# Optimization experiments

Measured on AMD Instinct MI355X. Metric: run time of the kernel, lower is better.

## Reference

```python
import jax, jax.numpy as jnp
import numpy as np
import itertools

NODE_DIM = 30
NUM_FEAT = 64
EDGE_DIM = NODE_DIM * NODE_DIM  # 900
D_IN, HID, LAT = 1024, 2048, 256
OUT_DIM = EDGE_DIM + NODE_DIM * NUM_FEAT  # 2820

_opt_nodes = [20, 21, 22, 23, 24, 25, 26, 27, 28, 29]
_opt_edges = [(i, j) for i, j in itertools.product(_opt_nodes, _opt_nodes) if i <= j]  # 55
_log_nodes = [20, 21, 22, 23, 24, 25, 26, 27, 28, 29, 14, 15]
_log_edges = [(i, j) for i, j in itertools.product(_log_nodes, _log_nodes) if i <= j]  # 78
N_OPT_NODES = len(_opt_nodes)          # 10
N_OPT_EDGES = len(_opt_edges)          # 55
N_LOG_NODES = len(_log_nodes)          # 12 (softmax width; only first 10 applied)
N_LOG_EDGES = len(_log_edges)          # 78 (softmax width; only first 55 applied)
OPT_NODES = jnp.array(_opt_nodes)
E0 = jnp.array([e[0] for e in _opt_edges])
E1 = jnp.array([e[1] for e in _opt_edges])


def _bn(x, g, b, m, v):
    # eval-mode BatchNorm1d, eps=1e-5
    return (x - m) * jax.lax.rsqrt(v + 1e-5) * g + b


def _attn_mlp(x, W1, b1, W2, b2):
    return jnp.tanh(x @ W1 + b1) @ W2 + b2


def _apply_attention(node_repr, edge_repr, node_w, edge_w):
    # softmax over full weight width, but indices always come from the optical lists
    nw = jax.nn.softmax(node_w, axis=1)[:, :N_OPT_NODES]   # [B,10]
    ew = jax.nn.softmax(edge_w, axis=1)[:, :N_OPT_EDGES]   # [B,55]
    node_repr = node_repr.at[:, OPT_NODES, :].set(node_repr[:, OPT_NODES, :] * nw[:, :, None])
    edge_repr = edge_repr.at[:, E0, E1].set(edge_repr[:, E0, E1] * ew)
    return node_repr, edge_repr


def setup_inputs() -> dict:
    key = jax.random.key(0)
    ks = iter(jax.random.split(key, 64))
    B = 8192
    s = 0.02
    def W(shape):
        return jax.random.normal(next(ks), shape, dtype=jnp.float32) * s
    inp = {
        "x": jax.random.normal(next(ks), (B, D_IN), dtype=jnp.float32),
        "optical": jax.random.normal(next(ks), (B, D_IN), dtype=jnp.float32),
        "log": jax.random.normal(next(ks), (B, D_IN), dtype=jnp.float32),
        "enc_W": W((D_IN, HID)), "enc_b": W((HID,)),
        "bn1_g": jnp.ones((HID,)), "bn1_b": jnp.zeros((HID,)),
        "bn1_m": W((HID,)), "bn1_v": jax.random.uniform(next(ks), (HID,)) + 0.5,
        "mu_W": W((HID, LAT)), "mu_b": W((LAT,)),
        "lv_W": W((HID, LAT)), "lv_b": W((LAT,)),
        "dec_W1": W((LAT, HID)), "dec_b1": W((HID,)),
        "bn2_g": jnp.ones((HID,)), "bn2_b": jnp.zeros((HID,)),
        "bn2_m": W((HID,)), "bn2_v": jax.random.uniform(next(ks), (HID,)) + 0.5,
        "dec_W2": W((HID, OUT_DIM)), "dec_b2": W((OUT_DIM,)),
        "on_W1": W((D_IN, D_IN // 2)), "on_b1": W((D_IN // 2,)),
        "on_W2": W((D_IN // 2, N_OPT_NODES)), "on_b2": W((N_OPT_NODES,)),
        "oe_W1": W((D_IN, D_IN // 2)), "oe_b1": W((D_IN // 2,)),
        "oe_W2": W((D_IN // 2, N_OPT_EDGES)), "oe_b2": W((N_OPT_EDGES,)),
        "ln_W1": W((D_IN, D_IN // 2)), "ln_b1": W((D_IN // 2,)),
        "ln_W2": W((D_IN // 2, N_LOG_NODES)), "ln_b2": W((N_LOG_NODES,)),
        "le_W1": W((D_IN, D_IN // 2)), "le_b1": W((D_IN // 2,)),
        "le_W2": W((D_IN // 2, N_LOG_EDGES)), "le_b2": W((N_LOG_EDGES,)),
    }
    return inp


def reference(x, optical, log, enc_W, enc_b, bn1_g, bn1_b, bn1_m, bn1_v,
              mu_W, mu_b, lv_W, lv_b, dec_W1, dec_b1, bn2_g, bn2_b, bn2_m, bn2_v,
              dec_W2, dec_b2, on_W1, on_b1, on_W2, on_b2, oe_W1, oe_b1, oe_W2, oe_b2,
              ln_W1, ln_b1, ln_W2, ln_b2, le_W1, le_b1, le_W2, le_b2):
    # encode (Linear -> ReLU -> BatchNorm(eval) -> Dropout(identity))
    h1 = _bn(jax.nn.relu(x @ enc_W + enc_b), bn1_g, bn1_b, bn1_m, bn1_v)
    mu = h1 @ mu_W + mu_b
    logvar = h1 @ lv_W + lv_b
    z = mu  # eval-mode reparameterize
    # decode
    h2 = _bn(jax.nn.relu(z @ dec_W1 + dec_b1), bn2_g, bn2_b, bn2_m, bn2_v)
    out = h2 @ dec_W2 + dec_b2
    edge_repr = out[:, :EDGE_DIM].reshape(-1, NODE_DIM, NODE_DIM)
    node_repr = out[:, EDGE_DIM:].reshape(-1, NODE_DIM, NUM_FEAT)
    # optical attention
    onw = _attn_mlp(optical, on_W1, on_b1, on_W2, on_b2)
    oew = _attn_mlp(optical, oe_W1, oe_b1, oe_W2, oe_b2)
    node_repr, edge_repr = _apply_attention(node_repr, edge_repr, onw, oew)
    # log attention (wider softmax, same indices — faithful to original code)
    lnw = _attn_mlp(log, ln_W1, ln_b1, ln_W2, ln_b2)
    lew = _attn_mlp(log, le_W1, le_b1, le_W2, le_b2)
    node_repr, edge_repr = _apply_attention(node_repr, edge_repr, lnw, lew)
    return edge_repr, node_repr, mu, logvar
```

## Files before the change

kernel.cpp:

```cpp
#include <hip/hip_runtime.h>

using u16 = unsigned short;
using u32 = unsigned int;

typedef __attribute__((ext_vector_type(8))) short bf16x8;
typedef __attribute__((ext_vector_type(4))) float f32x4;

__device__ __forceinline__ u16 f2bf(float f) {
  u32 u = __float_as_uint(f);
  u += 0x7fffu + ((u >> 16) & 1u);
  return (u16)(u >> 16);
}
__device__ __forceinline__ float bf2f(u16 h) { return __uint_as_float(((u32)h) << 16); }

__device__ __forceinline__ void gld16(const u16* g, u16* s) {
  __builtin_amdgcn_global_load_lds((const __attribute__((address_space(1))) u32*)g,
                                   (__attribute__((address_space(3))) u32*)s, 16, 0, 0);
}

struct EpParams {
  const float* bias;
  const float* bnsc;
  const float* bnsh;
  u16* dhi; u16* dlo; int dstride;
  float* f32a; float* f32b; int f32stride;
  const float* nscale; const float* escale;
};

template<int EP, int NM, bool SLO>
__global__ __launch_bounds__(256, (NM == 1) ? 3 : 2) void gemm_k(
    const u16* __restrict__ Ah, const u16* __restrict__ Al, int lda,
    const u16* __restrict__ Bh, const u16* __restrict__ Bl,
    int K, int N, EpParams p)
{
  __shared__ __align__(16) u16 sAh[4096], sBh[4096];
  __shared__ __align__(16) u16 sAl[(NM >= 2) ? 4096 : 16];
  __shared__ __align__(16) u16 sBl[(NM == 3) ? 4096 : 16];
  const int t = threadIdx.x;
  const int lane = t & 63, wid = t >> 6;
  const int tm = blockIdx.x, tn = blockIdx.y;

  const int rp = t >> 2, sp = t & 3;
  const int rl = (rp & ~1) | ((rp & 1) ^ ((rp >> 2) & 1));
  const int sl = sp ^ (rl & 3);
  const u16* pAh = Ah + (size_t)(tm * 128 + rl) * (size_t)lda + sl * 8;
  const u16* pBh = Bh + (size_t)(tn * 128 + rl) * (size_t)K + sl * 8;
  const u16* pAl = (NM >= 2) ? Al + (size_t)(tm * 128 + rl) * (size_t)lda + sl * 8 : pAh;
  const u16* pBl = (NM == 3) ? Bl + (size_t)(tn * 128 + rl) * (size_t)K + sl * 8 : pBh;
  const size_t aStep = (size_t)64 * (size_t)lda;
  const size_t bStep = (size_t)64 * (size_t)K;

  f32x4 acc[4][4];
#pragma unroll
  for (int m = 0; m < 4; m++)
#pragma unroll
    for (int n = 0; n < 4; n++) acc[m][n] = f32x4{0.f, 0.f, 0.f, 0.f};

  const int fr = lane & 15, fg = lane >> 4;
  const int wm = wid >> 1, wn = wid & 1;

  for (int kk = 0; kk < K; kk += 32) {
    gld16(pAh + kk,          sAh + wid * 512);
    gld16(pAh + aStep + kk,  sAh + 2048 + wid * 512);
    gld16(pBh + kk,          sBh + wid * 512);
    gld16(pBh + bStep + kk,  sBh + 2048 + wid * 512);
    if constexpr (NM >= 2) {
      gld16(pAl + kk,         sAl + wid * 512);
      gld16(pAl + aStep + kk, sAl + 2048 + wid * 512);
    }
    if constexpr (NM == 3) {
      gld16(pBl + kk,         sBl + wid * 512);
      gld16(pBl + bStep + kk, sBl + 2048 + wid * 512);
    }
    __syncthreads();

    bf16x8 a_h[4], b_h[4], a_l[4], b_l[4];
#pragma unroll
    for (int f = 0; f < 4; f++) {
      const int ar = wm * 64 + f * 16 + fr;
      const int br = wn * 64 + f * 16 + fr;
      a_h[f] = *(const bf16x8*)&sAh[(ar * 32 + fg * 8) ^ ((ar & 7) << 3)];
      b_h[f] = *(const bf16x8*)&sBh[(br * 32 + fg * 8) ^ ((br & 7) << 3)];
      if constexpr (NM >= 2) a_l[f] = *(const bf16x8*)&sAl[(ar * 32 + fg * 8) ^ ((ar & 7) << 3)];
      if constexpr (NM == 3) b_l[f] = *(const bf16x8*)&sBl[(br * 32 + fg * 8) ^ ((br & 7) << 3)];
    }
#pragma unroll
    for (int m = 0; m < 4; m++)
#pragma unroll
      for (int n = 0; n < 4; n++) {
        if constexpr (NM == 3)
          acc[m][n] = __builtin_amdgcn_mfma_f32_16x16x32_bf16(a_h[m], b_l[n], acc[m][n], 0, 0, 0);
        if constexpr (NM >= 2)
          acc[m][n] = __builtin_amdgcn_mfma_f32_16x16x32_bf16(a_l[m], b_h[n], acc[m][n], 0, 0, 0);
        acc[m][n] = __builtin_amdgcn_mfma_f32_16x16x32_bf16(a_h[m], b_h[n], acc[m][n], 0, 0, 0);
      }
    __syncthreads();
  }

  const int rowb = tm * 128 + wm * 64;
  const int colb = tn * 128 + wn * 64;
#pragma unroll
  for (int n = 0; n < 4; n++) {
    const int col = colb + n * 16 + fr;
#pragma unroll
    for (int m = 0; m < 4; m++) {
#pragma unroll
      for (int r = 0; r < 4; r++) {
        const int row = rowb + m * 16 + fg * 4 + r;
        float val = acc[m][n][r];
        if constexpr (EP == 0) {
          val += p.bias[col];
          val = fmaxf(val, 0.f);
          val = val * p.bnsc[col] + p.bnsh[col];
          u16 h = f2bf(val);
          p.dhi[(size_t)row * p.dstride + col] = h;
          if constexpr (SLO)
            p.dlo[(size_t)row * p.dstride + col] = f2bf(val - bf2f(h));
        } else if constexpr (EP == 1) {
          val += p.bias[col];
          if (col < 256) {
            p.f32a[(size_t)row * 256 + col] = val;
            u16 h = f2bf(val);
            p.dhi[(size_t)row * 256 + col] = h;
            p.dlo[(size_t)row * 256 + col] = f2bf(val - bf2f(h));
          } else {
            p.f32b[(size_t)row * 256 + (col - 256)] = val;
          }
        } else if constexpr (EP == 2) {
          val = tanhf(val + p.bias[col]);
          p.dhi[(size_t)row * p.dstride + col] = f2bf(val);
        } else if constexpr (EP == 3) {
          if (col < N) p.f32a[(size_t)row * p.f32stride + col] = val + p.bias[col];
        } else {
          if (col < N) {
            val += p.bias[col];
            if (col < 900) {
              int rr = col / 30, cc = col - rr * 30;
              float s = 1.f;
              if (rr >= 20 && cc >= 20 && rr <= cc) {
                int i0 = rr - 20, j0 = cc - 20;
                int k = i0 * 10 - ((i0 * (i0 - 1)) >> 1) + (j0 - i0);
                s = p.escale[(size_t)row * 55 + k];
              }
              p.f32a[(size_t)row * 900 + col] = val * s;
            } else {
              int tc = col - 900, rr = tc >> 6;
              float s = (rr >= 20) ? p.nscale[(size_t)row * 10 + (rr - 20)] : 1.f;
              p.f32b[(size_t)row * 1920 + tc] = val * s;
            }
          }
        }
      }
    }
  }
}

__global__ void conv3(const float* __restrict__ x, const float* __restrict__ opt,
                      const float* __restrict__ lg, u16* __restrict__ xh,
                      u16* __restrict__ xl, u16* __restrict__ oh, u16* __restrict__ lh) {
  const int SEG = 8192 * 1024 / 4;
  int i = blockIdx.x * blockDim.x + threadIdx.x;
  if (i < SEG) {
    float4 v = ((const float4*)x)[i];
    ushort4 hh, ll;
    hh.x = f2bf(v.x); ll.x = f2bf(v.x - bf2f(hh.x));
    hh.y = f2bf(v.y); ll.y = f2bf(v.y - bf2f(hh.y));
    hh.z = f2bf(v.z); ll.z = f2bf(v.z - bf2f(hh.z));
    hh.w = f2bf(v.w); ll.w = f2bf(v.w - bf2f(hh.w));
    ((ushort4*)xh)[i] = hh;
    ((ushort4*)xl)[i] = ll;
  } else if (i < 2 * SEG) {
    int j = i - SEG;
    float4 v = ((const float4*)opt)[j];
    ushort4 hh;
    hh.x = f2bf(v.x); hh.y = f2bf(v.y); hh.z = f2bf(v.z); hh.w = f2bf(v.w);
    ((ushort4*)oh)[j] = hh;
  } else if (i < 3 * SEG) {
    int j = i - 2 * SEG;
    float4 v = ((const float4*)lg)[j];
    ushort4 hh;
    hh.x = f2bf(v.x); hh.y = f2bf(v.y); hh.z = f2bf(v.z); hh.w = f2bf(v.w);
    ((ushort4*)lh)[j] = hh;
  }
}

__global__ void conv_wT(const float* __restrict__ W, u16* __restrict__ Th,
                        u16* __restrict__ Tl, int K, int N) {
  __shared__ float tile[32][33];
  int k0 = blockIdx.x * 32, n0 = blockIdx.y * 32;
  int tx = threadIdx.x, ty = threadIdx.y;
#pragma unroll
  for (int i = ty; i < 32; i += 8) {
    int n = n0 + tx;
    tile[i][tx] = (n < N) ? W[(size_t)(k0 + i) * N + n] : 0.f;
  }
  __syncthreads();
#pragma unroll
  for (int i = ty; i < 32; i += 8) {
    int n = n0 + i, k = k0 + tx;
    float v = tile[tx][i];
    u16 h = f2bf(v);
    Th[(size_t)n * K + k] = h;
    if (Tl) Tl[(size_t)n * K + k] = f2bf(v - bf2f(h));
  }
}

__global__ void conv_w2bd(const float* __restrict__ Wa, int Na,
                          const float* __restrict__ Wb, int Nb,
                          u16* __restrict__ Th) {
  int idx = blockIdx.x * blockDim.x + threadIdx.x;
  if (idx >= 128 * 1024) return;
  int n = idx >> 10, k = idx & 1023;
  float v = 0.f;
  if (n < Na) { if (k < 512) v = Wa[(size_t)k * Na + n]; }
  else if (n < Na + Nb) { if (k >= 512) v = Wb[(size_t)(k - 512) * Nb + (n - Na)]; }
  Th[idx] = f2bf(v);
}

struct PrepArgs {
  const float *bn1_g, *bn1_b, *bn1_m, *bn1_v, *bn2_g, *bn2_b, *bn2_m, *bn2_v;
  const float *mu_b, *lv_b, *on_b1, *oe_b1, *ln_b1, *le_b1, *on_b2, *oe_b2, *ln_b2, *le_b2;
  float *bn1sc, *bn1sh, *bn2sc, *bn2sh, *bias_mulv, *bias_o1, *bias_l1, *bias_o2, *bias_l2;
};
__global__ void prep_k(PrepArgs a) {
  int i = blockIdx.x * blockDim.x + threadIdx.x;
  if (i < 2048) {
    float s = a.bn1_g[i] * rsqrtf(a.bn1_v[i] + 1e-5f);
    a.bn1sc[i] = s; a.bn1sh[i] = a.bn1_b[i] - a.bn1_m[i] * s;
  } else if (i < 4096) {
    int j = i - 2048;
    float s = a.bn2_g[j] * rsqrtf(a.bn2_v[j] + 1e-5f);
    a.bn2sc[j] = s; a.bn2sh[j] = a.bn2_b[j] - a.bn2_m[j] * s;
  } else if (i < 4608) {
    int j = i - 4096; a.bias_mulv[j] = (j < 256) ? a.mu_b[j] : a.lv_b[j - 256];
  } else if (i < 5632) {
    int j = i - 4608; a.bias_o1[j] = (j < 512) ? a.on_b1[j] : a.oe_b1[j - 512];
  } else if (i < 6656) {
    int j = i - 5632; a.bias_l1[j] = (j < 512) ? a.ln_b1[j] : a.le_b1[j - 512];
  } else if (i < 6721) {
    int j = i - 6656; a.bias_o2[j] = (j < 10) ? a.on_b2[j] : a.oe_b2[j - 10];
  } else if (i < 6811) {
    int j = i - 6721; a.bias_l2[j] = (j < 12) ? a.ln_b2[j] : a.le_b2[j - 12];
  }
}

__global__ void softmax_combine(const float* __restrict__ lo, const float* __restrict__ ll,
                                float* __restrict__ nsc, float* __restrict__ esc) {
  int b = blockIdx.x * blockDim.x + threadIdx.x;
  if (b >= 8192) return;
  const float* po = lo + (size_t)b * 65;
  const float* pl = ll + (size_t)b * 90;
  float mo = po[0];
  for (int i = 1; i < 10; i++) mo = fmaxf(mo, po[i]);
  float so = 0.f;
  for (int i = 0; i < 10; i++) so += expf(po[i] - mo);
  float ml = pl[0];
  for (int i = 1; i < 12; i++) ml = fmaxf(ml, pl[i]);
  float sl = 0.f;
  for (int i = 0; i < 12; i++) sl += expf(pl[i] - ml);
  float invn = 1.f / (so * sl);
  for (int i = 0; i < 10; i++)
    nsc[(size_t)b * 10 + i] = expf(po[i] - mo) * expf(pl[i] - ml) * invn;
  const float* qo = po + 10;
  const float* ql = pl + 12;
  float meo = qo[0];
  for (int i = 1; i < 55; i++) meo = fmaxf(meo, qo[i]);
  float seo = 0.f;
  for (int i = 0; i < 55; i++) seo += expf(qo[i] - meo);
  float mel = ql[0];
  for (int i = 1; i < 78; i++) mel = fmaxf(mel, ql[i]);
  float sel = 0.f;
  for (int i = 0; i < 78; i++) sel += expf(ql[i] - mel);
  float inve = 1.f / (seo * sel);
  for (int k = 0; k < 55; k++)
    esc[(size_t)b * 55 + k] = expf(qo[k] - meo) * expf(ql[k] - mel) * inve;
}

extern "C" void kernel_launch(void* const* d_in, const int* in_sizes, int n_in,
                              void* d_out, int out_size, void* d_ws, size_t ws_size,
                              hipStream_t stream) {
  const float* x       = (const float*)d_in[0];
  const float* optical = (const float*)d_in[1];
  const float* logx    = (const float*)d_in[2];
  const float* enc_W   = (const float*)d_in[3];
  const float* enc_b   = (const float*)d_in[4];
  const float* bn1_g   = (const float*)d_in[5];
  const float* bn1_b   = (const float*)d_in[6];
  const float* bn1_m   = (const float*)d_in[7];
  const float* bn1_v   = (const float*)d_in[8];
  const float* mu_W    = (const float*)d_in[9];
  const float* mu_b    = (const float*)d_in[10];
  const float* lv_W    = (const float*)d_in[11];
  const float* lv_b    = (const float*)d_in[12];
  const float* dec_W1  = (const float*)d_in[13];
  const float* dec_b1  = (const float*)d_in[14];
  const float* bn2_g   = (const float*)d_in[15];
  const float* bn2_b   = (const float*)d_in[16];
  const float* bn2_m   = (const float*)d_in[17];
  const float* bn2_v   = (const float*)d_in[18];
  const float* dec_W2  = (const float*)d_in[19];
  const float* dec_b2  = (const float*)d_in[20];
  const float* on_W1   = (const float*)d_in[21];
  const float* on_b1   = (const float*)d_in[22];
  const float* on_W2   = (const float*)d_in[23];
  const float* on_b2   = (const float*)d_in[24];
  const float* oe_W1   = (const float*)d_in[25];
  const float* oe_b1   = (const float*)d_in[26];
  const float* oe_W2   = (const float*)d_in[27];
  const float* oe_b2   = (const float*)d_in[28];
  const float* ln_W1   = (const float*)d_in[29];
  const float* ln_b1   = (const float*)d_in[30];
  const float* ln_W2   = (const float*)d_in[31];
  const float* ln_b2   = (const float*)d_in[32];
  const float* le_W1   = (const float*)d_in[33];
  const float* le_b1   = (const float*)d_in[34];
  const float* le_W2   = (const float*)d_in[35];
  const float* le_b2   = (const float*)d_in[36];

  const int B = 8192;
  float* out_edge = (float*)d_out;
  float* out_node = out_edge + (size_t)B * 900;
  float* out_mu   = out_node + (size_t)B * 1920;
  float* out_lv   = out_mu + (size_t)B * 256;

  char* base = (char*)d_ws;
  size_t off = 0;
  auto takeB = [&](size_t elems) -> u16* {
    u16* p = (u16*)(base + off);
    off = (off + elems * 2 + 255) & ~(size_t)255;
    return p;
  };
  auto takeF = [&](size_t elems) -> float* {
    float* p = (float*)(base + off);
    off = (off + elems * 4 + 255) & ~(size_t)255;
    return p;
  };
  u16* wEncH  = takeB(2048 * 1024);
  u16* wMulvH = takeB(512 * 2048);   u16* wMulvL = takeB(512 * 2048);
  u16* wDec1H = takeB(2048 * 256);   u16* wDec1L = takeB(2048 * 256);
  u16* wDec2H = takeB(2944 * 2048);
  u16* wO1H   = takeB(1024 * 1024);
  u16* wL1H   = takeB(1024 * 1024);
  u16* wO2H   = takeB(128 * 1024);
  u16* wL2H   = takeB(128 * 1024);
  u16* aXh = takeB((size_t)B * 1024); u16* aXl = takeB((size_t)B * 1024);
  u16* aOh = takeB((size_t)B * 1024);
  u16* aLh = takeB((size_t)B * 1024);
  u16* aHh = takeB((size_t)B * 2048); u16* aHl = takeB((size_t)B * 2048);
  u16* aZh = takeB((size_t)B * 256);  u16* aZl = takeB((size_t)B * 256);
  u16* aTh = takeB((size_t)B * 2048);
  float* logitsO = takeF((size_t)B * 65);
  float* logitsL = takeF((size_t)B * 90);
  float* nsc = takeF((size_t)B * 10);
  float* esc = takeF((size_t)B * 55);
  float* bn1sc = takeF(2048); float* bn1sh = takeF(2048);
  float* bn2sc = takeF(2048); float* bn2sh = takeF(2048);
  float* bias_mulv = takeF(512);
  float* bias_o1 = takeF(1024);
  float* bias_l1 = takeF(1024);
  float* bias_o2 = takeF(65);
  float* bias_l2 = takeF(90);

  PrepArgs pa;
  pa.bn1_g = bn1_g; pa.bn1_b = bn1_b; pa.bn1_m = bn1_m; pa.bn1_v = bn1_v;
  pa.bn2_g = bn2_g; pa.bn2_b = bn2_b; pa.bn2_m = bn2_m; pa.bn2_v = bn2_v;
  pa.mu_b = mu_b; pa.lv_b = lv_b;
  pa.on_b1 = on_b1; pa.oe_b1 = oe_b1; pa.ln_b1 = ln_b1; pa.le_b1 = le_b1;
  pa.on_b2 = on_b2; pa.oe_b2 = oe_b2; pa.ln_b2 = ln_b2; pa.le_b2 = le_b2;
  pa.bn1sc = bn1sc; pa.bn1sh = bn1sh; pa.bn2sc = bn2sc; pa.bn2sh = bn2sh;
  pa.bias_mulv = bias_mulv; pa.bias_o1 = bias_o1; pa.bias_l1 = bias_l1;
  pa.bias_o2 = bias_o2; pa.bias_l2 = bias_l2;
  prep_k<<<27, 256, 0, stream>>>(pa);

  conv3<<<24576, 256, 0, stream>>>(x, optical, logx, aXh, aXl, aOh, aLh);

  dim3 tb(32, 8);
  conv_wT<<<dim3(32, 64), tb, 0, stream>>>(enc_W, wEncH, nullptr, 1024, 2048);
  conv_wT<<<dim3(64, 8), tb, 0, stream>>>(mu_W, wMulvH, wMulvL, 2048, 256);
  conv_wT<<<dim3(64, 8), tb, 0, stream>>>(
      lv_W, wMulvH + (size_t)256 * 2048, wMulvL + (size_t)256 * 2048, 2048, 256);
  conv_wT<<<dim3(8, 64), tb, 0, stream>>>(dec_W1, wDec1H, wDec1L, 256, 2048);
  conv_wT<<<dim3(64, 92), tb, 0, stream>>>(dec_W2, wDec2H, nullptr, 2048, 2820);
  conv_wT<<<dim3(32, 16), tb, 0, stream>>>(on_W1, wO1H, nullptr, 1024, 512);
  conv_wT<<<dim3(32, 16), tb, 0, stream>>>(oe_W1, wO1H + (size_t)512 * 1024, nullptr, 1024, 512);
  conv_wT<<<dim3(32, 16), tb, 0, stream>>>(ln_W1, wL1H, nullptr, 1024, 512);
  conv_wT<<<dim3(32, 16), tb, 0, stream>>>(le_W1, wL1H + (size_t)512 * 1024, nullptr, 1024, 512);
  conv_w2bd<<<512, 256, 0, stream>>>(on_W2, 10, oe_W2, 55, wO2H);
  conv_w2bd<<<512, 256, 0, stream>>>(ln_W2, 12, le_W2, 78, wL2H);

  EpParams p;

  p = EpParams{};
  p.bias = enc_b; p.bnsc = bn1sc; p.bnsh = bn1sh;
  p.dhi = aHh; p.dlo = aHl; p.dstride = 2048;
  gemm_k<0, 2, true><<<dim3(64, 16), 256, 0, stream>>>(
      aXh, aXl, 1024, wEncH, nullptr, 1024, 2048, p);

  p = EpParams{};
  p.bias = bias_mulv; p.f32a = out_mu; p.f32b = out_lv;
  p.dhi = aZh; p.dlo = aZl; p.dstride = 256;
  gemm_k<1, 3, false><<<dim3(64, 4), 256, 0, stream>>>(
      aHh, aHl, 2048, wMulvH, wMulvL, 2048, 512, p);

  p = EpParams{};
  p.bias = dec_b1; p.bnsc = bn2sc; p.bnsh = bn2sh;
  p.dhi = aHh; p.dlo = nullptr; p.dstride = 2048;
  gemm_k<0, 3, false><<<dim3(64, 16), 256, 0, stream>>>(
      aZh, aZl, 256, wDec1H, wDec1L, 256, 2048, p);

  p = EpParams{};
  p.bias = bias_o1; p.dhi = aTh; p.dstride = 2048;
  gemm_k<2, 1, false><<<dim3(64, 8), 256, 0, stream>>>(
      aOh, nullptr, 1024, wO1H, nullptr, 1024, 1024, p);
  p.bias = bias_l1; p.dhi = aTh + 1024;
  gemm_k<2, 1, false><<<dim3(64, 8), 256, 0, stream>>>(
      aLh, nullptr, 1024, wL1H, nullptr, 1024, 1024, p);

  p = EpParams{};
  p.bias = bias_o2; p.f32a = logitsO; p.f32stride = 65;
  gemm_k<3, 1, false><<<dim3(64, 1), 256, 0, stream>>>(
      aTh, nullptr, 2048, wO2H, nullptr, 1024, 65, p);
  p.bias = bias_l2; p.f32a = logitsL; p.f32stride = 90;
  gemm_k<3, 1, false><<<dim3(64, 1), 256, 0, stream>>>(
      aTh + 1024, nullptr, 2048, wL2H, nullptr, 1024, 90, p);

  softmax_combine<<<32, 256, 0, stream>>>(logitsO, logitsL, nsc, esc);

  p = EpParams{};
  p.bias = dec_b2; p.nscale = nsc; p.escale = esc;
  p.f32a = out_edge; p.f32b = out_node;
  gemm_k<4, 1, false><<<dim3(64, 23), 256, 0, stream>>>(
      aHh, nullptr, 2048, wDec2H, nullptr, 2048, 2820, p);
}
```

Baseline: 861.8 us.

## Add 256x256 triple-buffered GEMM kernel and batch attention GEMMs into single launches

Adds a new 512-thread GEMM kernel with 256x256 output tiles and a three-slot LDS ring. Global-to-LDS loads are interleaved between two half-tile MFMA phases with raised wave priority. It replaces the encoder, attention-hidden and decoder-output GEMMs, and merges the optical/log attention GEMMs of both layers into single launches that pick weights and bias by block index. The aim is more data reuse per tile, loads overlapped with compute, and fewer launches. The cost is padding the decoder weight to 3072 rows, larger LDS use, and fragile hand-written waitcnt counting.

```diff
diff --git a/kernel.cpp b/kernel.cpp
--- a/kernel.cpp
+++ b/kernel.cpp
@@ -5,6 +5,8 @@
 
 typedef __attribute__((ext_vector_type(8))) short bf16x8;
 typedef __attribute__((ext_vector_type(4))) float f32x4;
+
+#define MFMA16 __builtin_amdgcn_mfma_f32_16x16x32_bf16
 
 __device__ __forceinline__ u16 f2bf(float f) {
   u32 u = __float_as_uint(f);
@@ -20,12 +22,182 @@
 
 struct EpParams {
   const float* bias;
+  const float* bias2;
+  const u16* b2;
   const float* bnsc;
   const float* bnsh;
   u16* dhi; u16* dlo; int dstride;
   float* f32a; float* f32b; int f32stride;
   const float* nscale; const float* escale;
 };
+
+template<int EP, int NM, bool SLO>
+__global__ __launch_bounds__(512, 2) void gemm256_k(
+    const u16* __restrict__ Ah, const u16* __restrict__ Al, int lda,
+    const u16* __restrict__ Bh, int K, int N, EpParams p)
+{
+  __shared__ __align__(16) u16 sA[3][8192];
+  __shared__ __align__(16) u16 sB[3][8192];
+  __shared__ __align__(16) u16 sAl[(NM >= 2) ? 3 : 1][8192];
+
+  const int t = threadIdx.x;
+  const int lane = t & 63, wid = t >> 6;
+  const int wm = wid >> 2, wn = wid & 3;
+  const int fr = lane & 15, fg = lane >> 4;
+  const int tm = blockIdx.x, tn = blockIdx.y;
+  const int NT = K >> 5;
+
+  const u16* BhS = Bh;
+  const float* bias = p.bias;
+  if constexpr (EP == 2) {
+    if (tm >= 32) { BhS = p.b2; bias = p.bias2; }
+  }
+
+  const int strow = wid * 16 + fr;
+  const u16* gA  = Ah + (size_t)(tm * 256 + strow) * (size_t)lda + fg * 8;
+  const u16* gAl = (NM >= 2) ? Al + (size_t)(tm * 256 + strow) * (size_t)lda + fg * 8 : gA;
+  const u16* gB  = BhS + (size_t)(tn * 256 + strow) * (size_t)K + fg * 8;
+
+  auto stA = [&](int slot, int c, int k0) {
+    gld16(gA + (size_t)c * 128 * lda + k0, &sA[slot][c * 4096 + wid * 512]);
+  };
+  auto stL = [&](int slot, int c, int k0) {
+    gld16(gAl + (size_t)c * 128 * lda + k0, &sAl[slot][c * 4096 + wid * 512]);
+  };
+  auto stB = [&](int slot, int c, int k0) {
+    gld16(gB + (size_t)c * 128 * K + k0, &sB[slot][c * 4096 + wid * 512]);
+  };
+
+  f32x4 acc[8][4];
+#pragma unroll
+  for (int m = 0; m < 8; m++)
+#pragma unroll
+    for (int n = 0; n < 4; n++) acc[m][n] = f32x4{0.f, 0.f, 0.f, 0.f};
+
+  stA(0, 0, 0); stA(0, 1, 0);
+  if constexpr (NM >= 2) { stL(0, 0, 0); stL(0, 1, 0); }
+  stB(0, 0, 0); stB(0, 1, 0);
+  stA(1, 0, 32); stA(1, 1, 32);
+  if constexpr (NM >= 2) { stL(1, 0, 32); stL(1, 1, 32); }
+  stB(1, 0, 32); stB(1, 1, 32);
+  if constexpr (NM >= 2) asm volatile("s_waitcnt vmcnt(6)" ::: "memory");
+  else                   asm volatile("s_waitcnt vmcnt(4)" ::: "memory");
+  __builtin_amdgcn_s_barrier();
+  __builtin_amdgcn_sched_barrier(0);
+
+  for (int tt = 0; tt < NT; ++tt) {
+    const int slot = tt % 3;
+    const int nsl  = (tt + 2) % 3;
+    const int k2   = (tt + 2) << 5;
+    const bool SG  = (tt + 2 < NT);
+    const u16* sa  = sA[slot];
+    const u16* sb  = sB[slot];
+    const u16* sal = sAl[(NM >= 2) ? slot : 0];
+
+    bf16x8 bfr[4], ah[4], al[4];
+#pragma unroll
+    for (int n = 0; n < 4; ++n) bfr[n] = *(const bf16x8*)&sb[(wn * 4 + n) * 512 + lane * 8];
+#pragma unroll
+    for (int m = 0; m < 4; ++m) ah[m] = *(const bf16x8*)&sa[(wm * 8 + m) * 512 + lane * 8];
+    if constexpr (NM >= 2) {
+#pragma unroll
+      for (int m = 0; m < 4; ++m) al[m] = *(const bf16x8*)&sal[(wm * 8 + m) * 512 + lane * 8];
+    }
+    if (SG) {
+      stA(nsl, 0, k2); stA(nsl, 1, k2);
+      if constexpr (NM >= 2) stL(nsl, 0, k2);
+    }
+    __builtin_amdgcn_s_barrier();
+    __builtin_amdgcn_sched_barrier(0);
+    __builtin_amdgcn_s_setprio(1);
+#pragma unroll
+    for (int m = 0; m < 4; ++m)
+#pragma unroll
+      for (int n = 0; n < 4; ++n) {
+        if constexpr (NM >= 2) acc[m][n] = MFMA16(al[m], bfr[n], acc[m][n], 0, 0, 0);
+        acc[m][n] = MFMA16(ah[m], bfr[n], acc[m][n], 0, 0, 0);
+      }
+    __builtin_amdgcn_s_setprio(0);
+    __builtin_amdgcn_s_barrier();
+    __builtin_amdgcn_sched_barrier(0);
+#pragma unroll
+    for (int m = 0; m < 4; ++m) ah[m] = *(const bf16x8*)&sa[(wm * 8 + 4 + m) * 512 + lane * 8];
+    if constexpr (NM >= 2) {
+#pragma unroll
+      for (int m = 0; m < 4; ++m) al[m] = *(const bf16x8*)&sal[(wm * 8 + 4 + m) * 512 + lane * 8];
+    }
+    if (SG) {
+      if constexpr (NM >= 2) stL(nsl, 1, k2);
+      stB(nsl, 0, k2); stB(nsl, 1, k2);
+    }
+    __builtin_amdgcn_s_barrier();
+    __builtin_amdgcn_sched_barrier(0);
+    __builtin_amdgcn_s_setprio(1);
+#pragma unroll
+    for (int m = 0; m < 4; ++m)
+#pragma unroll
+      for (int n = 0; n < 4; ++n) {
+        if constexpr (NM >= 2) acc[4 + m][n] = MFMA16(al[m], bfr[n], acc[4 + m][n], 0, 0, 0);
+        acc[4 + m][n] = MFMA16(ah[m], bfr[n], acc[4 + m][n], 0, 0, 0);
+      }
+    __builtin_amdgcn_s_setprio(0);
+    asm volatile("s_waitcnt lgkmcnt(0)" ::: "memory");
+    __builtin_amdgcn_sched_barrier(0);
+    if (SG) {
+      if constexpr (NM >= 2) asm volatile("s_waitcnt vmcnt(6)" ::: "memory");
+      else                   asm volatile("s_waitcnt vmcnt(4)" ::: "memory");
+    } else {
+      asm volatile("s_waitcnt vmcnt(0)" ::: "memory");
+    }
+    __builtin_amdgcn_s_barrier();
+    __builtin_amdgcn_sched_barrier(0);
+  }
+
+  const int rowb = tm * 256 + wm * 128;
+  const int colb = tn * 256 + wn * 64;
+#pragma unroll
+  for (int n = 0; n < 4; ++n) {
+    const int col = colb + n * 16 + fr;
+#pragma unroll
+    for (int m = 0; m < 8; ++m) {
+#pragma unroll
+      for (int r = 0; r < 4; ++r) {
+        const int row = rowb + m * 16 + fg * 4 + r;
+        float val = acc[m][n][r];
+        if constexpr (EP == 0) {
+          val += bias[col];
+          val = fmaxf(val, 0.f);
+          val = val * p.bnsc[col] + p.bnsh[col];
+          u16 h = f2bf(val);
+          p.dhi[(size_t)row * p.dstride + col] = h;
+          if constexpr (SLO)
+            p.dlo[(size_t)row * p.dstride + col] = f2bf(val - bf2f(h));
+        } else if constexpr (EP == 2) {
+          val = tanhf(val + bias[col]);
+          p.dhi[(size_t)row * p.dstride + col] = f2bf(val);
+        } else {
+          if (col < N) {
+            val += bias[col];
+            if (col < 900) {
+              int rr = col / 30, cc = col - rr * 30;
+              float s = 1.f;
+              if (rr >= 20 && cc >= 20 && rr <= cc) {
+                int i0 = rr - 20, j0 = cc - 20;
+                int k = i0 * 10 - ((i0 * (i0 - 1)) >> 1) + (j0 - i0);
+                s = p.escale[(size_t)row * 55 + k];
+              }
+              p.f32a[(size_t)row * 900 + col] = val * s;
+            } else {
+              int tc = col - 900, rr = tc >> 6;
+              float s = (rr >= 20) ? p.nscale[(size_t)row * 10 + (rr - 20)] : 1.f;
+              p.f32b[(size_t)row * 1920 + tc] = val * s;
+            }
+          }
+        }
+      }
+    }
+  }
+}
 
 template<int EP, int NM, bool SLO>
 __global__ __launch_bounds__(256, (NM == 1) ? 3 : 2) void gemm_k(
@@ -40,11 +212,14 @@
   const int lane = t & 63, wid = t >> 6;
   const int tm = blockIdx.x, tn = blockIdx.y;
 
+  const u16* BhS = Bh;
+  if constexpr (EP == 5) { if (tm >= 64) BhS = p.b2; }
+
   const int rp = t >> 2, sp = t & 3;
   const int rl = (rp & ~1) | ((rp & 1) ^ ((rp >> 2) & 1));
   const int sl = sp ^ (rl & 3);
   const u16* pAh = Ah + (size_t)(tm * 128 + rl) * (size_t)lda + sl * 8;
-  const u16* pBh = Bh + (size_t)(tn * 128 + rl) * (size_t)K + sl * 8;
+  const u16* pBh = BhS + (size_t)(tn * 128 + rl) * (size_t)K + sl * 8;
   const u16* pAl = (NM >= 2) ? Al + (size_t)(tm * 128 + rl) * (size_t)lda + sl * 8 : pAh;
   const u16* pBl = (NM == 3) ? Bl + (size_t)(tn * 128 + rl) * (size_t)K + sl * 8 : pBh;
   const size_t aStep = (size_t)64 * (size_t)lda;
@@ -89,10 +264,10 @@
 #pragma unroll
       for (int n = 0; n < 4; n++) {
         if constexpr (NM == 3)
-          acc[m][n] = __builtin_amdgcn_mfma_f32_16x16x32_bf16(a_h[m], b_l[n], acc[m][n], 0, 0, 0);
+          acc[m][n] = MFMA16(a_h[m], b_l[n], acc[m][n], 0, 0, 0);
         if constexpr (NM >= 2)
-          acc[m][n] = __builtin_amdgcn_mfma_f32_16x16x32_bf16(a_l[m], b_h[n], acc[m][n], 0, 0, 0);
-        acc[m][n] = __builtin_amdgcn_mfma_f32_16x16x32_bf16(a_h[m], b_h[n], acc[m][n], 0, 0, 0);
+          acc[m][n] = MFMA16(a_l[m], b_h[n], acc[m][n], 0, 0, 0);
+        acc[m][n] = MFMA16(a_h[m], b_h[n], acc[m][n], 0, 0, 0);
       }
     __syncthreads();
   }
@@ -126,28 +301,11 @@
           } else {
             p.f32b[(size_t)row * 256 + (col - 256)] = val;
           }
-        } else if constexpr (EP == 2) {
-          val = tanhf(val + p.bias[col]);
-          p.dhi[(size_t)row * p.dstride + col] = f2bf(val);
-        } else if constexpr (EP == 3) {
-          if (col < N) p.f32a[(size_t)row * p.f32stride + col] = val + p.bias[col];
-        } else {
-          if (col < N) {
-            val += p.bias[col];
-            if (col < 900) {
-              int rr = col / 30, cc = col - rr * 30;
-              float s = 1.f;
-              if (rr >= 20 && cc >= 20 && rr <= cc) {
-                int i0 = rr - 20, j0 = cc - 20;
-                int k = i0 * 10 - ((i0 * (i0 - 1)) >> 1) + (j0 - i0);
-                s = p.escale[(size_t)row * 55 + k];
-              }
-              p.f32a[(size_t)row * 900 + col] = val * s;
-            } else {
-              int tc = col - 900, rr = tc >> 6;
-              float s = (rr >= 20) ? p.nscale[(size_t)row * 10 + (rr - 20)] : 1.f;
-              p.f32b[(size_t)row * 1920 + tc] = val * s;
-            }
+        } else if constexpr (EP == 5) {
+          if (tm < 64) {
+            if (col < 65) p.f32a[(size_t)row * 65 + col] = val + p.bias[col];
+          } else {
+            if (col < 90) p.f32b[(size_t)(row - 8192) * 90 + col] = val + p.bias2[col];
           }
         }
       }
@@ -338,17 +496,18 @@
   u16* wEncH  = takeB(2048 * 1024);
   u16* wMulvH = takeB(512 * 2048);   u16* wMulvL = takeB(512 * 2048);
   u16* wDec1H = takeB(2048 * 256);   u16* wDec1L = takeB(2048 * 256);
-  u16* wDec2H = takeB(2944 * 2048);
+  u16* wDec2H = takeB(3072 * 2048);
   u16* wO1H   = takeB(1024 * 1024);
   u16* wL1H   = takeB(1024 * 1024);
   u16* wO2H   = takeB(128 * 1024);
   u16* wL2H   = takeB(128 * 1024);
   u16* aXh = takeB((size_t)B * 1024); u16* aXl = takeB((size_t)B * 1024);
-  u16* aOh = takeB((size_t)B * 1024);
-  u16* aLh = takeB((size_t)B * 1024);
+  u16* aOLh = takeB((size_t)2 * B * 1024);
+  u16* aOh = aOLh;
+  u16* aLh = aOLh + (size_t)B * 1024;
   u16* aHh = takeB((size_t)B * 2048); u16* aHl = takeB((size_t)B * 2048);
   u16* aZh = takeB((size_t)B * 256);  u16* aZl = takeB((size_t)B * 256);
-  u16* aTh = takeB((size_t)B * 2048);
+  u16* aTh = takeB((size_t)2 * B * 1024);
   float* logitsO = takeF((size_t)B * 65);
   float* logitsL = takeF((size_t)B * 90);
   float* nsc = takeF((size_t)B * 10);
@@ -380,7 +539,7 @@
   conv_wT<<<dim3(64, 8), tb, 0, stream>>>(
       lv_W, wMulvH + (size_t)256 * 2048, wMulvL + (size_t)256 * 2048, 2048, 256);
   conv_wT<<<dim3(8, 64), tb, 0, stream>>>(dec_W1, wDec1H, wDec1L, 256, 2048);
-  conv_wT<<<dim3(64, 92), tb, 0, stream>>>(dec_W2, wDec2H, nullptr, 2048, 2820);
+  conv_wT<<<dim3(64, 96), tb, 0, stream>>>(dec_W2, wDec2H, nullptr, 2048, 2820);
   conv_wT<<<dim3(32, 16), tb, 0, stream>>>(on_W1, wO1H, nullptr, 1024, 512);
   conv_wT<<<dim3(32, 16), tb, 0, stream>>>(oe_W1, wO1H + (size_t)512 * 1024, nullptr, 1024, 512);
   conv_wT<<<dim3(32, 16), tb, 0, stream>>>(ln_W1, wL1H, nullptr, 1024, 512);
@@ -393,8 +552,8 @@
   p = EpParams{};
   p.bias = enc_b; p.bnsc = bn1sc; p.bnsh = bn1sh;
   p.dhi = aHh; p.dlo = aHl; p.dstride = 2048;
-  gemm_k<0, 2, true><<<dim3(64, 16), 256, 0, stream>>>(
-      aXh, aXl, 1024, wEncH, nullptr, 1024, 2048, p);
+  gemm256_k<0, 2, true><<<dim3(32, 8), 512, 0, stream>>>(
+      aXh, aXl, 1024, wEncH, 1024, 2048, p);
 
   p = EpParams{};
   p.bias = bias_mulv; p.f32a = out_mu; p.f32b = out_lv;
@@ -409,26 +568,22 @@
       aZh, aZl, 256, wDec1H, wDec1L, 256, 2048, p);
 
   p = EpParams{};
-  p.bias = bias_o1; p.dhi = aTh; p.dstride = 2048;
-  gemm_k<2, 1, false><<<dim3(64, 8), 256, 0, stream>>>(
-      aOh, nullptr, 1024, wO1H, nullptr, 1024, 1024, p);
-  p.bias = bias_l1; p.dhi = aTh + 1024;
-  gemm_k<2, 1, false><<<dim3(64, 8), 256, 0, stream>>>(
-      aLh, nullptr, 1024, wL1H, nullptr, 1024, 1024, p);
+  p.bias = bias_o1; p.bias2 = bias_l1; p.b2 = wL1H;
+  p.dhi = aTh; p.dstride = 1024;
+  gemm256_k<2, 1, false><<<dim3(64, 4), 512, 0, stream>>>(
+      aOLh, nullptr, 1024, wO1H, 1024, 1024, p);
 
   p = EpParams{};
-  p.bias = bias_o2; p.f32a = logitsO; p.f32stride = 65;
-  gemm_k<3, 1, false><<<dim3(64, 1), 256, 0, stream>>>(
-      aTh, nullptr, 2048, wO2H, nullptr, 1024, 65, p);
-  p.bias = bias_l2; p.f32a = logitsL; p.f32stride = 90;
-  gemm_k<3, 1, false><<<dim3(64, 1), 256, 0, stream>>>(
-      aTh + 1024, nullptr, 2048, wL2H, nullptr, 1024, 90, p);
+  p.bias = bias_o2; p.bias2 = bias_l2; p.b2 = wL2H;
+  p.f32a = logitsO; p.f32b = logitsL;
+  gemm_k<5, 1, false><<<dim3(128, 1), 256, 0, stream>>>(
+      aTh, nullptr, 1024, wO2H, nullptr, 1024, 128, p);
 
   softmax_combine<<<32, 256, 0, stream>>>(logitsO, logitsL, nsc, esc);
 
   p = EpParams{};
   p.bias = dec_b2; p.nscale = nsc; p.escale = esc;
   p.f32a = out_edge; p.f32b = out_node;
-  gemm_k<4, 1, false><<<dim3(64, 23), 256, 0, stream>>>(
-      aHh, nullptr, 2048, wDec2H, nullptr, 2048, 2820, p);
-}
+  gemm256_k<4, 1, false><<<dim3(32, 12), 512, 0, stream>>>(
+      aHh, nullptr, 2048, wDec2H, 2048, 2820, p);
+}
```

Result: slower. 880.0 us (+2.1%).

## Drop weight low-bf16 terms, merge attention GEMM launches and weight transposes

Applied to the files above, without the earlier changes.

Stops computing the low-order bf16 split of the mu/logvar and dec_W1 weights, so those GEMMs run two MFMA passes instead of three and the weight conversion writes only the high half. The optical and log attention GEMMs (both layers) are merged into single launches with a doubled M grid, where the upper half of the blocks selects the second weight and bias. All weight transposes are batched into one kernel driven by a job table. This cuts launch count and MFMA work, at some cost in accuracy on the mu/logvar and decoder-hidden paths.

```diff
diff --git a/kernel.cpp b/kernel.cpp
--- a/kernel.cpp
+++ b/kernel.cpp
@@ -5,6 +5,8 @@
 
 typedef __attribute__((ext_vector_type(8))) short bf16x8;
 typedef __attribute__((ext_vector_type(4))) float f32x4;
+
+#define MFMA16 __builtin_amdgcn_mfma_f32_16x16x32_bf16
 
 __device__ __forceinline__ u16 f2bf(float f) {
   u32 u = __float_as_uint(f);
@@ -20,6 +22,8 @@
 
 struct EpParams {
   const float* bias;
+  const float* bias2;
+  const u16* b2;
   const float* bnsc;
   const float* bnsh;
   u16* dhi; u16* dlo; int dstride;
@@ -40,11 +44,17 @@
   const int lane = t & 63, wid = t >> 6;
   const int tm = blockIdx.x, tn = blockIdx.y;
 
+  const u16* BhS = Bh;
+  const float* bias = p.bias;
+  if constexpr (EP == 2 || EP == 5) {
+    if (tm >= 64) { BhS = p.b2; bias = p.bias2; }
+  }
+
   const int rp = t >> 2, sp = t & 3;
   const int rl = (rp & ~1) | ((rp & 1) ^ ((rp >> 2) & 1));
   const int sl = sp ^ (rl & 3);
   const u16* pAh = Ah + (size_t)(tm * 128 + rl) * (size_t)lda + sl * 8;
-  const u16* pBh = Bh + (size_t)(tn * 128 + rl) * (size_t)K + sl * 8;
+  const u16* pBh = BhS + (size_t)(tn * 128 + rl) * (size_t)K + sl * 8;
   const u16* pAl = (NM >= 2) ? Al + (size_t)(tm * 128 + rl) * (size_t)lda + sl * 8 : pAh;
   const u16* pBl = (NM == 3) ? Bl + (size_t)(tn * 128 + rl) * (size_t)K + sl * 8 : pBh;
   const size_t aStep = (size_t)64 * (size_t)lda;
@@ -89,10 +99,10 @@
 #pragma unroll
       for (int n = 0; n < 4; n++) {
         if constexpr (NM == 3)
-          acc[m][n] = __builtin_amdgcn_mfma_f32_16x16x32_bf16(a_h[m], b_l[n], acc[m][n], 0, 0, 0);
+          acc[m][n] = MFMA16(a_h[m], b_l[n], acc[m][n], 0, 0, 0);
         if constexpr (NM >= 2)
-          acc[m][n] = __builtin_amdgcn_mfma_f32_16x16x32_bf16(a_l[m], b_h[n], acc[m][n], 0, 0, 0);
-        acc[m][n] = __builtin_amdgcn_mfma_f32_16x16x32_bf16(a_h[m], b_h[n], acc[m][n], 0, 0, 0);
+          acc[m][n] = MFMA16(a_l[m], b_h[n], acc[m][n], 0, 0, 0);
+        acc[m][n] = MFMA16(a_h[m], b_h[n], acc[m][n], 0, 0, 0);
       }
     __syncthreads();
   }
@@ -109,7 +119,7 @@
         const int row = rowb + m * 16 + fg * 4 + r;
         float val = acc[m][n][r];
         if constexpr (EP == 0) {
-          val += p.bias[col];
+          val += bias[col];
           val = fmaxf(val, 0.f);
           val = val * p.bnsc[col] + p.bnsh[col];
           u16 h = f2bf(val);
@@ -117,7 +127,7 @@
           if constexpr (SLO)
             p.dlo[(size_t)row * p.dstride + col] = f2bf(val - bf2f(h));
         } else if constexpr (EP == 1) {
-          val += p.bias[col];
+          val += bias[col];
           if (col < 256) {
             p.f32a[(size_t)row * 256 + col] = val;
             u16 h = f2bf(val);
@@ -127,13 +137,17 @@
             p.f32b[(size_t)row * 256 + (col - 256)] = val;
           }
         } else if constexpr (EP == 2) {
-          val = tanhf(val + p.bias[col]);
+          val = tanhf(val + bias[col]);
           p.dhi[(size_t)row * p.dstride + col] = f2bf(val);
-        } else if constexpr (EP == 3) {
-          if (col < N) p.f32a[(size_t)row * p.f32stride + col] = val + p.bias[col];
+        } else if constexpr (EP == 5) {
+          if (tm < 64) {
+            if (col < 65) p.f32a[(size_t)row * 65 + col] = val + bias[col];
+          } else {
+            if (col < 90) p.f32b[(size_t)(row - 8192) * 90 + col] = val + bias[col];
+          }
         } else {
           if (col < N) {
-            val += p.bias[col];
+            val += bias[col];
             if (col < 900) {
               int rr = col / 30, cc = col - rr * 30;
               float s = 1.f;
@@ -184,24 +198,29 @@
   }
 }
 
-__global__ void conv_wT(const float* __restrict__ W, u16* __restrict__ Th,
-                        u16* __restrict__ Tl, int K, int N) {
+struct WTJob { const float* src; u16* dh; int K, N, nbx, blk0; };
+struct WTJobs { WTJob j[9]; };
+__global__ void conv_wT_all(WTJobs J) {
   __shared__ float tile[32][33];
-  int k0 = blockIdx.x * 32, n0 = blockIdx.y * 32;
-  int tx = threadIdx.x, ty = threadIdx.y;
+  const int b = blockIdx.x;
+  int ji = 0;
+#pragma unroll
+  for (int q = 1; q < 9; q++) if (b >= J.j[q].blk0) ji = q;
+  const WTJob jb = J.j[ji];
+  const int bl = b - jb.blk0;
+  const int kb = bl % jb.nbx, nb = bl / jb.nbx;
+  const int k0 = kb * 32, n0 = nb * 32;
+  const int tx = threadIdx.x, ty = threadIdx.y;
 #pragma unroll
   for (int i = ty; i < 32; i += 8) {
     int n = n0 + tx;
-    tile[i][tx] = (n < N) ? W[(size_t)(k0 + i) * N + n] : 0.f;
+    tile[i][tx] = (n < jb.N) ? jb.src[(size_t)(k0 + i) * jb.N + n] : 0.f;
   }
   __syncthreads();
 #pragma unroll
   for (int i = ty; i < 32; i += 8) {
     int n = n0 + i, k = k0 + tx;
-    float v = tile[tx][i];
-    u16 h = f2bf(v);
-    Th[(size_t)n * K + k] = h;
-    if (Tl) Tl[(size_t)n * K + k] = f2bf(v - bf2f(h));
+    jb.dh[(size_t)n * jb.K + k] = f2bf(tile[tx][i]);
   }
 }
 
@@ -336,19 +355,20 @@
     return p;
   };
   u16* wEncH  = takeB(2048 * 1024);
-  u16* wMulvH = takeB(512 * 2048);   u16* wMulvL = takeB(512 * 2048);
-  u16* wDec1H = takeB(2048 * 256);   u16* wDec1L = takeB(2048 * 256);
+  u16* wMulvH = takeB(512 * 2048);
+  u16* wDec1H = takeB(2048 * 256);
   u16* wDec2H = takeB(2944 * 2048);
   u16* wO1H   = takeB(1024 * 1024);
   u16* wL1H   = takeB(1024 * 1024);
   u16* wO2H   = takeB(128 * 1024);
   u16* wL2H   = takeB(128 * 1024);
   u16* aXh = takeB((size_t)B * 1024); u16* aXl = takeB((size_t)B * 1024);
-  u16* aOh = takeB((size_t)B * 1024);
-  u16* aLh = takeB((size_t)B * 1024);
+  u16* aOLh = takeB((size_t)2 * B * 1024);
+  u16* aOh = aOLh;
+  u16* aLh = aOLh + (size_t)B * 1024;
   u16* aHh = takeB((size_t)B * 2048); u16* aHl = takeB((size_t)B * 2048);
   u16* aZh = takeB((size_t)B * 256);  u16* aZl = takeB((size_t)B * 256);
-  u16* aTh = takeB((size_t)B * 2048);
+  u16* aTh = takeB((size_t)2 * B * 1024);
   float* logitsO = takeF((size_t)B * 65);
   float* logitsL = takeF((size_t)B * 90);
   float* nsc = takeF((size_t)B * 10);
@@ -374,17 +394,22 @@
 
   conv3<<<24576, 256, 0, stream>>>(x, optical, logx, aXh, aXl, aOh, aLh);
 
-  dim3 tb(32, 8);
-  conv_wT<<<dim3(32, 64), tb, 0, stream>>>(enc_W, wEncH, nullptr, 1024, 2048);
-  conv_wT<<<dim3(64, 8), tb, 0, stream>>>(mu_W, wMulvH, wMulvL, 2048, 256);
-  conv_wT<<<dim3(64, 8), tb, 0, stream>>>(
-      lv_W, wMulvH + (size_t)256 * 2048, wMulvL + (size_t)256 * 2048, 2048, 256);
-  conv_wT<<<dim3(8, 64), tb, 0, stream>>>(dec_W1, wDec1H, wDec1L, 256, 2048);
-  conv_wT<<<dim3(64, 92), tb, 0, stream>>>(dec_W2, wDec2H, nullptr, 2048, 2820);
-  conv_wT<<<dim3(32, 16), tb, 0, stream>>>(on_W1, wO1H, nullptr, 1024, 512);
-  conv_wT<<<dim3(32, 16), tb, 0, stream>>>(oe_W1, wO1H + (size_t)512 * 1024, nullptr, 1024, 512);
-  conv_wT<<<dim3(32, 16), tb, 0, stream>>>(ln_W1, wL1H, nullptr, 1024, 512);
-  conv_wT<<<dim3(32, 16), tb, 0, stream>>>(le_W1, wL1H + (size_t)512 * 1024, nullptr, 1024, 512);
+  WTJobs wj;
+  int blk = 0;
+  auto addjob = [&](int idx, const float* src, u16* dh, int K, int N, int Npad) {
+    wj.j[idx] = WTJob{src, dh, K, N, K / 32, blk};
+    blk += (K / 32) * (Npad / 32);
+  };
+  addjob(0, enc_W,  wEncH,  1024, 2048, 2048);
+  addjob(1, mu_W,   wMulvH, 2048, 256, 256);
+  addjob(2, lv_W,   wMulvH + (size_t)256 * 2048, 2048, 256, 256);
+  addjob(3, dec_W1, wDec1H, 256, 2048, 2048);
+  addjob(4, dec_W2, wDec2H, 2048, 2820, 2944);
+  addjob(5, on_W1,  wO1H,                        1024, 512, 512);
+  addjob(6, oe_W1,  wO1H + (size_t)512 * 1024,   1024, 512, 512);
+  addjob(7, ln_W1,  wL1H,                        1024, 512, 512);
+  addjob(8, le_W1,  wL1H + (size_t)512 * 1024,   1024, 512, 512);
+  conv_wT_all<<<blk, dim3(32, 8), 0, stream>>>(wj);
   conv_w2bd<<<512, 256, 0, stream>>>(on_W2, 10, oe_W2, 55, wO2H);
   conv_w2bd<<<512, 256, 0, stream>>>(ln_W2, 12, le_W2, 78, wL2H);
 
@@ -399,30 +424,26 @@
   p = EpParams{};
   p.bias = bias_mulv; p.f32a = out_mu; p.f32b = out_lv;
   p.dhi = aZh; p.dlo = aZl; p.dstride = 256;
-  gemm_k<1, 3, false><<<dim3(64, 4), 256, 0, stream>>>(
-      aHh, aHl, 2048, wMulvH, wMulvL, 2048, 512, p);
+  gemm_k<1, 2, false><<<dim3(64, 4), 256, 0, stream>>>(
+      aHh, aHl, 2048, wMulvH, nullptr, 2048, 512, p);
 
   p = EpParams{};
   p.bias = dec_b1; p.bnsc = bn2sc; p.bnsh = bn2sh;
   p.dhi = aHh; p.dlo = nullptr; p.dstride = 2048;
-  gemm_k<0, 3, false><<<dim3(64, 16), 256, 0, stream>>>(
-      aZh, aZl, 256, wDec1H, wDec1L, 256, 2048, p);
-
-  p = EpParams{};
-  p.bias = bias_o1; p.dhi = aTh; p.dstride = 2048;
-  gemm_k<2, 1, false><<<dim3(64, 8), 256, 0, stream>>>(
-      aOh, nullptr, 1024, wO1H, nullptr, 1024, 1024, p);
-  p.bias = bias_l1; p.dhi = aTh + 1024;
-  gemm_k<2, 1, false><<<dim3(64, 8), 256, 0, stream>>>(
-      aLh, nullptr, 1024, wL1H, nullptr, 1024, 1024, p);
-
-  p = EpParams{};
-  p.bias = bias_o2; p.f32a = logitsO; p.f32stride = 65;
-  gemm_k<3, 1, false><<<dim3(64, 1), 256, 0, stream>>>(
-      aTh, nullptr, 2048, wO2H, nullptr, 1024, 65, p);
-  p.bias = bias_l2; p.f32a = logitsL; p.f32stride = 90;
-  gemm_k<3, 1, false><<<dim3(64, 1), 256, 0, stream>>>(
-      aTh + 1024, nullptr, 2048, wL2H, nullptr, 1024, 90, p);
+  gemm_k<0, 2, false><<<dim3(64, 16), 256, 0, stream>>>(
+      aZh, aZl, 256, wDec1H, nullptr, 256, 2048, p);
+
+  p = EpParams{};
+  p.bias = bias_o1; p.bias2 = bias_l1; p.b2 = wL1H;
+  p.dhi = aTh; p.dstride = 1024;
+  gemm_k<2, 1, false><<<dim3(128, 8), 256, 0, stream>>>(
+      aOLh, nullptr, 1024, wO1H, nullptr, 1024, 1024, p);
+
+  p = EpParams{};
+  p.bias = bias_o2; p.bias2 = bias_l2; p.b2 = wL2H;
+  p.f32a = logitsO; p.f32b = logitsL;
+  gemm_k<5, 1, false><<<dim3(128, 1), 256, 0, stream>>>(
+      aTh, nullptr, 1024, wO2H, nullptr, 1024, 128, p);
 
   softmax_combine<<<32, 256, 0, stream>>>(logitsO, logitsL, nsc, esc);
 
```

Measured after the change: 786.0 us. -8.8%, faster.
